# Performance work log

Hardware: AMD Instinct MI355X
Metric: run time of the kernel (lower is better)

## Reference

```python
import jax, jax.numpy as jnp
import numpy as np

B, S, C, V, LAT, NL = 256, 512, 256, 32, 256, 7
DILS = [1, 2, 4, 8, 16, 32, 64]
EPS = 1e-5


def setup_inputs() -> dict:
    key = jax.random.key(0)
    ks = jax.random.split(key, 24)
    s = 0.05
    inp = {
        "x": jax.random.randint(ks[0], (B, S), 0, V, dtype=jnp.int64 if jax.config.read("jax_enable_x64") else jnp.int32),
        "z": jax.random.normal(ks[1], (B, LAT), dtype=jnp.float32),
        "emb": jax.random.normal(ks[2], (V, C), dtype=jnp.float32) * s,
        "latent_W": jax.random.normal(ks[3], (LAT, C), dtype=jnp.float32) * s,
        "latent_b": jnp.zeros((C,), jnp.float32),
        "ln1_g": jnp.ones((NL, C), jnp.float32),
        "ln1_b": jnp.zeros((NL, C), jnp.float32),
        "w1": jax.random.normal(ks[4], (NL, C, C), jnp.float32) * s,
        "b1": jnp.zeros((NL, C), jnp.float32),
        "ln2_g": jnp.ones((NL, C), jnp.float32),
        "ln2_b": jnp.zeros((NL, C), jnp.float32),
        "wd": jax.random.normal(ks[5], (NL, 2, C, C), jnp.float32) * s,  # tap 0 = x[t-d], tap 1 = x[t]
        "bd": jnp.zeros((NL, C), jnp.float32),
        "ln3_g": jnp.ones((NL, C), jnp.float32),
        "ln3_b": jnp.zeros((NL, C), jnp.float32),
        "we": jax.random.normal(ks[6], (NL, C, C), jnp.float32) * s,
        "be": jnp.zeros((NL, C), jnp.float32),
        "wg": jax.random.normal(ks[7], (NL, C, C), jnp.float32) * s,
        "bg": jnp.zeros((NL, C), jnp.float32),
        "out_W": jax.random.normal(ks[8], (C, V), jnp.float32) * s,
        "out_b": jnp.zeros((V,), jnp.float32),
    }
    return inp


def _ln(h, g, b):
    mu = h.mean(-1, keepdims=True)
    var = jnp.mean((h - mu) ** 2, axis=-1, keepdims=True)
    return (h - mu) * jax.lax.rsqrt(var + EPS) * g + b


def _lrelu(h):
    return jnp.where(h >= 0, h, 0.01 * h)


def reference(x, z, emb, latent_W, latent_b, ln1_g, ln1_b, w1, b1,
              ln2_g, ln2_b, wd, bd, ln3_g, ln3_b, we, be, wg, bg,
              out_W, out_b):
    # channel-last layout [B, S, C] throughout (fuses away the torch transposes)
    h = emb[x] + (z @ latent_W + latent_b)[:, None, :]
    for i, d in enumerate(DILS):
        x_inp = h
        t = _lrelu(_ln(x_inp, ln1_g[i], ln1_b[i]))
        t = t @ w1[i] + b1[i]
        t = _lrelu(_ln(t, ln2_g[i], ln2_b[i]))
        # causal dilated conv, kernel=2: out[t] = W0*x[t-d] + W1*x[t]
        t_shift = jnp.pad(t, ((0, 0), (d, 0), (0, 0)))[:, :t.shape[1], :]
        t = t_shift @ wd[i, 0] + t @ wd[i, 1] + bd[i]
        t = _lrelu(_ln(t, ln3_g[i], ln3_b[i]))
        gated = (t @ we[i] + be[i]) * jax.nn.sigmoid(t @ wg[i] + bg[i])
        h = gated + x_inp
    logits = h @ out_W + out_b                      # [B, S, V]
    lp = jax.nn.log_softmax(logits, axis=-1)
    # gather log-prob of next token: lp[:, :-1, :] at x[:, 1:]
    return jnp.take_along_axis(lp[:, :-1, :], x[:, 1:, None], axis=2)[..., 0]
```

## Files before the change

kernel.cpp:

```cpp
#include <hip/hip_runtime.h>

typedef unsigned short u16;
typedef unsigned int   u32;
typedef __attribute__((ext_vector_type(8))) short short8;
typedef __attribute__((ext_vector_type(4))) float f32x4;

struct __align__(8) u16x4 { u16 x, y, z, w; };

#define NL 7
#define M_DIM 131072

#define VMW(N) asm volatile("s_waitcnt vmcnt(" #N ")" ::: "memory")
#define LGW()  asm volatile("s_waitcnt lgkmcnt(0)" ::: "memory")
#define BAR()  __builtin_amdgcn_s_barrier()

__device__ __forceinline__ float b2f(u16 u) {
  union { float f; u32 i; } c; c.i = ((u32)u) << 16; return c.f;
}
__device__ __forceinline__ u16 f2b(float f) {
  union { float f; u32 i; } c; c.f = f;
  u32 r = c.i + 0x7FFFu + ((c.i >> 16) & 1u);
  return (u16)(r >> 16);
}
__device__ __forceinline__ void gload16(const void* g, void* l) {
  __builtin_amdgcn_global_load_lds((const __attribute__((address_space(1))) void*)g,
                                   (__attribute__((address_space(3))) void*)l, 16, 0, 0);
}
__device__ __forceinline__ int xIdx(int row, int chunk) {
  return row * 256 + (((chunk) ^ (row & 7)) << 3);
}


__global__ __launch_bounds__(256) void conv_w1_k(const float* __restrict__ w1, u16* __restrict__ wT) {
  int idx = blockIdx.x * 256 + threadIdx.x;
  int i = idx >> 16, rem = idx & 65535;
  int n = rem >> 8, k = rem & 255;
  wT[idx] = f2b(w1[(i << 16) + (k << 8) + n]);
}

__global__ __launch_bounds__(256) void conv_wd_k(const float* __restrict__ wd, u16* __restrict__ wT) {
  int idx = blockIdx.x * 256 + threadIdx.x;
  int i = idx / 131072, rem = idx & 131071;
  int n = rem >> 9, k2 = rem & 511;
  int tap = k2 >> 8, k = k2 & 255;
  wT[idx] = f2b(wd[(((i * 2 + tap) << 8) + k) * 256 + n]);
}

__global__ __launch_bounds__(256) void conv_weg_k(const float* __restrict__ we, const float* __restrict__ wg,
                                                  u16* __restrict__ wT) {
  int idx = blockIdx.x * 256 + threadIdx.x;
  int i = idx / 131072, rem = idx & 131071;
  int src = rem >> 16, n = (rem >> 8) & 255, k = rem & 255;
  const float* W = src ? wg : we;
  wT[idx] = f2b(W[((i << 8) + k) * 256 + n]);
}

__global__ __launch_bounds__(256) void conv_wo_k(const float* __restrict__ outW, u16* __restrict__ wTo) {
  int idx = blockIdx.x * 256 + threadIdx.x;
  int v = idx >> 8, k = idx & 255;
  wTo[idx] = f2b(outW[k * 32 + v]);
}


__global__ __launch_bounds__(256) void zlat_k(const float* __restrict__ z, const float* __restrict__ W,
                                              const float* __restrict__ bias, float* __restrict__ zlat) {
  int b = blockIdx.x, c = threadIdx.x;
  float acc = bias[c];
  for (int l = 0; l < 256; ++l) acc += z[b * 256 + l] * W[l * 256 + c];
  zlat[b * 256 + c] = acc;
}


__global__ __launch_bounds__(256) void embed_k(const int* __restrict__ x, const float* __restrict__ emb,
                                               const float* __restrict__ zlat, u16* __restrict__ h) {
  int wave = threadIdx.x >> 6, lane = threadIdx.x & 63;
  int r = blockIdx.x * 4 + wave;
  int c = lane * 4;
  int tok = x[r];
  int bi = r >> 9;
  float4 ev = *(const float4*)&emb[tok * 256 + c];
  float4 zv = *(const float4*)&zlat[bi * 256 + c];
  u16x4 hb;
  hb.x = f2b(ev.x + zv.x); hb.y = f2b(ev.y + zv.y);
  hb.z = f2b(ev.z + zv.z); hb.w = f2b(ev.w + zv.w);
  *(u16x4*)&h[(long)r * 256 + c] = hb;
}


__global__ __launch_bounds__(256, 3) void gemm1_k(
    const u16* __restrict__ h, const u16* __restrict__ WT,
    const float* __restrict__ ln1g, const float* __restrict__ ln1b,
    const float* __restrict__ bias,
    const float* __restrict__ ln2g, const float* __restrict__ ln2b,
    u16* __restrict__ V)
{
  __shared__ __align__(16) u16 lA[64 * 256];
  __shared__ __align__(16) u16 lB[256 * 32];
  float* pS  = (float*)lB;
  float* pQ  = (float*)(lB + 512);
  float* muA = (float*)(lB + 1024);
  float* rsA = (float*)(lB + 1152);
  const int tid = threadIdx.x;
  const int lane = tid & 63;
  const int wv = tid >> 6;
  const int wc = wv * 64;
  const int m0 = blockIdx.x * 64;
  const int rA = tid >> 2;
  const int cSw = ((((tid & 3) - ((tid >> 3) & 3)) & 3)) * 8;
  const int lr = lane & 15;
  const int quad = lane >> 4;
  const int sw = ((quad + ((lr >> 1) & 3)) & 3) * 8;

  {
    const int half = lane >> 5, l5 = lane & 31;
    float4 ga = *(const float4*)&ln1g[l5 * 8];
    float4 gb = *(const float4*)&ln1g[l5 * 8 + 4];
    float4 ba = *(const float4*)&ln1b[l5 * 8];
    float4 bb = *(const float4*)&ln1b[l5 * 8 + 4];
    #pragma unroll 4
    for (int it = 0; it < 8; ++it) {
      int row = wv * 16 + it * 2 + half;
      uint4 hv = *(const uint4*)(h + (long)(m0 + row) * 256 + l5 * 8);
      float v0 = b2f((u16)(hv.x & 0xffff)), v1 = b2f((u16)(hv.x >> 16));
      float v2 = b2f((u16)(hv.y & 0xffff)), v3 = b2f((u16)(hv.y >> 16));
      float v4 = b2f((u16)(hv.z & 0xffff)), v5 = b2f((u16)(hv.z >> 16));
      float v6 = b2f((u16)(hv.w & 0xffff)), v7 = b2f((u16)(hv.w >> 16));
      float s = v0 + v1 + v2 + v3 + v4 + v5 + v6 + v7;
      float q = v0*v0 + v1*v1 + v2*v2 + v3*v3 + v4*v4 + v5*v5 + v6*v6 + v7*v7;
      #pragma unroll
      for (int o = 1; o < 32; o <<= 1) { s += __shfl_xor(s, o); q += __shfl_xor(q, o); }
      float mu = s * 0.00390625f;
      float var = q * 0.00390625f - mu * mu;
      float rs = rsqrtf(var + 1e-5f);
      float y0 = (v0 - mu) * rs * ga.x + ba.x; y0 = y0 >= 0.f ? y0 : 0.01f * y0;
      float y1 = (v1 - mu) * rs * ga.y + ba.y; y1 = y1 >= 0.f ? y1 : 0.01f * y1;
      float y2 = (v2 - mu) * rs * ga.z + ba.z; y2 = y2 >= 0.f ? y2 : 0.01f * y2;
      float y3 = (v3 - mu) * rs * ga.w + ba.w; y3 = y3 >= 0.f ? y3 : 0.01f * y3;
      float y4 = (v4 - mu) * rs * gb.x + bb.x; y4 = y4 >= 0.f ? y4 : 0.01f * y4;
      float y5 = (v5 - mu) * rs * gb.y + bb.y; y5 = y5 >= 0.f ? y5 : 0.01f * y5;
      float y6 = (v6 - mu) * rs * gb.z + bb.z; y6 = y6 >= 0.f ? y6 : 0.01f * y6;
      float y7 = (v7 - mu) * rs * gb.w + bb.w; y7 = y7 >= 0.f ? y7 : 0.01f * y7;
      uint4 ov;
      ov.x = (u32)f2b(y0) | ((u32)f2b(y1) << 16);
      ov.y = (u32)f2b(y2) | ((u32)f2b(y3) << 16);
      ov.z = (u32)f2b(y4) | ((u32)f2b(y5) << 16);
      ov.w = (u32)f2b(y6) | ((u32)f2b(y7) << 16);
      *(uint4*)&lA[xIdx(row, l5)] = ov;
    }
  }

  f32x4 acc[4][4];
  #pragma unroll
  for (int i = 0; i < 4; ++i)
    #pragma unroll
    for (int j = 0; j < 4; ++j) {
      acc[i][j][0] = 0.f; acc[i][j][1] = 0.f; acc[i][j][2] = 0.f; acc[i][j][3] = 0.f;
    }

  for (int kt = 0; kt < 8; ++kt) {
    const long bofs = (long)rA * 256 + kt * 32 + cSw;
    #pragma unroll
    for (int j = 0; j < 4; ++j)
      gload16(WT + bofs + (long)(64 * j) * 256, &lB[tid * 8 + j * 2048]);
    __syncthreads();

    short8 af[4], bfr[4];
    #pragma unroll
    for (int mt = 0; mt < 4; ++mt)
      af[mt] = *(const short8*)&lA[xIdx(mt * 16 + lr, 4 * kt + quad)];
    #pragma unroll
    for (int nt = 0; nt < 4; ++nt)
      bfr[nt] = *(const short8*)&lB[(wc + nt * 16 + lr) * 32 + sw];
    #pragma unroll
    for (int mt = 0; mt < 4; ++mt)
      #pragma unroll
      for (int nt = 0; nt < 4; ++nt)
        acc[mt][nt] = __builtin_amdgcn_mfma_f32_16x16x32_bf16(af[mt], bfr[nt], acc[mt][nt], 0, 0, 0);
    __syncthreads();
  }

  float biasv[4], gv[4], bv[4];
  #pragma unroll
  for (int nt = 0; nt < 4; ++nt) {
    int n = wc + nt * 16 + lr;
    biasv[nt] = bias[n]; gv[nt] = ln2g[n]; bv[nt] = ln2b[n];
  }
  #pragma unroll
  for (int mt = 0; mt < 4; ++mt)
    #pragma unroll
    for (int r = 0; r < 4; ++r) {
      float s = 0.f, q = 0.f;
      #pragma unroll
      for (int nt = 0; nt < 4; ++nt) {
        float v = acc[mt][nt][r] + biasv[nt];
        acc[mt][nt][r] = v;
        s += v; q += v * v;
      }
      #pragma unroll
      for (int o = 1; o < 16; o <<= 1) { s += __shfl_xor(s, o); q += __shfl_xor(q, o); }
      if (lr == 0) { pS[(mt * 16 + quad * 4 + r) * 4 + wv] = s; pQ[(mt * 16 + quad * 4 + r) * 4 + wv] = q; }
    }
  __syncthreads();
  if (tid < 64) {
    float S = pS[tid * 4 + 0] + pS[tid * 4 + 1] + pS[tid * 4 + 2] + pS[tid * 4 + 3];
    float Q = pQ[tid * 4 + 0] + pQ[tid * 4 + 1] + pQ[tid * 4 + 2] + pQ[tid * 4 + 3];
    float mu = S * 0.00390625f;
    float var = Q * 0.00390625f - mu * mu;
    muA[tid] = mu; rsA[tid] = rsqrtf(var + 1e-5f);
  }
  __syncthreads();
  #pragma unroll
  for (int mt = 0; mt < 4; ++mt)
    #pragma unroll
    for (int r = 0; r < 4; ++r) {
      int row = mt * 16 + quad * 4 + r;
      float mu = muA[row], rs = rsA[row];
      #pragma unroll
      for (int nt = 0; nt < 4; ++nt) {
        float y = (acc[mt][nt][r] - mu) * rs * gv[nt] + bv[nt];
        y = y >= 0.f ? y : 0.01f * y;
        V[(long)(m0 + row) * 256 + wc + nt * 16 + lr] = f2b(y);
      }
    }
}


__global__ __launch_bounds__(512, 2) void conv_gate_k(
    const u16* __restrict__ A,
    const u16* __restrict__ WTd,
    int dil,
    const float* __restrict__ bd3, const float* __restrict__ g3, const float* __restrict__ bb3,
    const u16* __restrict__ WTe, const u16* __restrict__ WTg,
    const float* __restrict__ bev_, const float* __restrict__ bgv_,
    u16* __restrict__ h)
{
  __shared__ __align__(16) u16 pT[128 * 256];
  __shared__ __align__(16) u16 stg[2][12288];
  float* pS  = (float*)stg[0];
  float* pQ  = (float*)(stg[0] + 1024);
  float* muA = (float*)(stg[0] + 2048);
  float* rsA = (float*)(stg[0] + 2304);

  const int tid = threadIdx.x;
  const int lane = tid & 63;
  const int wv = tid >> 6;
  const int mw = wv >> 2;
  const int nw = wv & 3;
  const int rb = mw * 64;
  const int wc = nw * 64;
  const int m0 = blockIdx.x * 128;
  const int rA = tid >> 2;
  const int cSw = ((((tid & 3) - ((tid >> 3) & 3)) & 3)) * 8;
  const int lr = lane & 15;
  const int quad = lane >> 4;
  const int sw = ((quad + ((lr >> 1) & 3)) & 3) * 8;
  const int mm = m0 + rA;
  const int s1 = mm & 511;
  const short8 zero8 = {0, 0, 0, 0, 0, 0, 0, 0};

  bool zz[4];
  #pragma unroll
  for (int mt = 0; mt < 4; ++mt)
    zz[mt] = ((m0 + rb + mt * 16 + lr) & 511) < dil;

#define STAGE1(KT, BB) do {                                                   \
    const int kt_ = (KT);                                                     \
    const int kk_ = (kt_ & 7) * 32;                                           \
    const int rr_ = (kt_ < 8 && s1 >= dil) ? (mm - dil) : mm;                 \
    gload16(A + (long)rr_ * 256 + kk_ + cSw, &stg[BB][tid * 8]);              \
    const u16* bS_ = WTd + kt_ * 32 + cSw;                                    \
    gload16(bS_ + (long)rA * 512,         &stg[BB][4096 + tid * 8]);          \
    gload16(bS_ + (long)(rA + 128) * 512, &stg[BB][8192 + tid * 8]);          \
  } while (0)
#define STAGEW(WP, KT, BB) do {                                               \
    const long bofs_ = (long)rA * 256 + (KT) * 32 + cSw;                      \
    gload16((WP) + bofs_,              &stg[BB][4096 + tid * 8]);             \
    gload16((WP) + bofs_ + 128L * 256, &stg[BB][8192 + tid * 8]);             \
  } while (0)

  f32x4 acc[4][4];
  #pragma unroll
  for (int i = 0; i < 4; ++i)
    #pragma unroll
    for (int j = 0; j < 4; ++j) {
      acc[i][j][0] = 0.f; acc[i][j][1] = 0.f; acc[i][j][2] = 0.f; acc[i][j][3] = 0.f;
    }

  STAGE1(0, 0);
  STAGE1(1, 1);
  VMW(3);
  BAR();

  #pragma unroll
  for (int r = 0; r < 16; ++r) {
    const int bb = r & 1;
    short8 af[4], bfr[4];
    #pragma unroll
    for (int mt = 0; mt < 4; ++mt) {
      af[mt] = *(const short8*)&stg[bb][(rb + mt * 16 + lr) * 32 + sw];
      if (r < 8 && zz[mt]) af[mt] = zero8;
    }
    #pragma unroll
    for (int nt = 0; nt < 4; ++nt)
      bfr[nt] = *(const short8*)&stg[bb][4096 + (wc + nt * 16 + lr) * 32 + sw];
    LGW();
    BAR();
    if (r <= 13)      STAGE1(r + 2, bb);
    else if (r == 14) STAGEW(WTe, 0, 0);
    else              STAGEW(WTe, 1, 1);
    #pragma unroll
    for (int mt = 0; mt < 4; ++mt)
      #pragma unroll
      for (int nt = 0; nt < 4; ++nt)
        acc[mt][nt] = __builtin_amdgcn_mfma_f32_16x16x32_bf16(af[mt], bfr[nt], acc[mt][nt], 0, 0, 0);
    if (r <= 13)      VMW(3);
    else if (r == 14) VMW(2);
    BAR();
  }

  float b3v[4], g3v[4], o3v[4];
  #pragma unroll
  for (int nt = 0; nt < 4; ++nt) {
    int n = wc + nt * 16 + lr;
    b3v[nt] = bd3[n]; g3v[nt] = g3[n]; o3v[nt] = bb3[n];
  }
  #pragma unroll
  for (int mt = 0; mt < 4; ++mt)
    #pragma unroll
    for (int r = 0; r < 4; ++r) {
      float s = 0.f, q = 0.f;
      #pragma unroll
      for (int nt = 0; nt < 4; ++nt) {
        float v = acc[mt][nt][r] + b3v[nt];
        acc[mt][nt][r] = v;
        s += v; q += v * v;
      }
      #pragma unroll
      for (int o = 1; o < 16; o <<= 1) { s += __shfl_xor(s, o); q += __shfl_xor(q, o); }
      if (lr == 0) {
        int row = rb + mt * 16 + quad * 4 + r;
        pS[row * 4 + nw] = s; pQ[row * 4 + nw] = q;
      }
    }
  LGW(); BAR();
  if (tid < 128) {
    float S = pS[tid * 4 + 0] + pS[tid * 4 + 1] + pS[tid * 4 + 2] + pS[tid * 4 + 3];
    float Q = pQ[tid * 4 + 0] + pQ[tid * 4 + 1] + pQ[tid * 4 + 2] + pQ[tid * 4 + 3];
    float mu = S * 0.00390625f;
    float var = Q * 0.00390625f - mu * mu;
    muA[tid] = mu; rsA[tid] = rsqrtf(var + 1e-5f);
  }
  LGW(); BAR();
  #pragma unroll
  for (int mt = 0; mt < 4; ++mt)
    #pragma unroll
    for (int r = 0; r < 4; ++r) {
      int row = rb + mt * 16 + quad * 4 + r;
      float mu = muA[row], rs = rsA[row];
      #pragma unroll
      for (int nt = 0; nt < 4; ++nt) {
        int col = wc + nt * 16 + lr;
        float y = (acc[mt][nt][r] - mu) * rs * g3v[nt] + o3v[nt];
        y = y >= 0.f ? y : 0.01f * y;
        pT[xIdx(row, col >> 3) + (col & 7)] = f2b(y);
      }
    }
  LGW(); VMW(2); BAR();

  f32x4 accE[4][4], accG[4][4];
  #pragma unroll
  for (int i = 0; i < 4; ++i)
    #pragma unroll
    for (int j = 0; j < 4; ++j) {
      accE[i][j][0] = 0.f; accE[i][j][1] = 0.f; accE[i][j][2] = 0.f; accE[i][j][3] = 0.f;
      accG[i][j][0] = 0.f; accG[i][j][1] = 0.f; accG[i][j][2] = 0.f; accG[i][j][3] = 0.f;
    }

  #pragma unroll
  for (int k = 0; k < 8; ++k) {
    const int bb = k & 1;
    short8 paf[4], bfe[4];
    #pragma unroll
    for (int mt = 0; mt < 4; ++mt)
      paf[mt] = *(const short8*)&pT[xIdx(rb + mt * 16 + lr, 4 * k + quad)];
    #pragma unroll
    for (int nt = 0; nt < 4; ++nt)
      bfe[nt] = *(const short8*)&stg[bb][4096 + (wc + nt * 16 + lr) * 32 + sw];
    LGW(); BAR();
    if (k <= 5)      STAGEW(WTe, k + 2, bb);
    else if (k == 6) STAGEW(WTg, 0, 0);
    else             STAGEW(WTg, 1, 1);
    #pragma unroll
    for (int mt = 0; mt < 4; ++mt)
      #pragma unroll
      for (int nt = 0; nt < 4; ++nt)
        accE[mt][nt] = __builtin_amdgcn_mfma_f32_16x16x32_bf16(paf[mt], bfe[nt], accE[mt][nt], 0, 0, 0);
    VMW(2);
    BAR();
  }

  #pragma unroll
  for (int k = 0; k < 8; ++k) {
    const int bb = k & 1;
    short8 paf[4], bfg[4];
    #pragma unroll
    for (int mt = 0; mt < 4; ++mt)
      paf[mt] = *(const short8*)&pT[xIdx(rb + mt * 16 + lr, 4 * k + quad)];
    #pragma unroll
    for (int nt = 0; nt < 4; ++nt)
      bfg[nt] = *(const short8*)&stg[bb][4096 + (wc + nt * 16 + lr) * 32 + sw];
    LGW(); BAR();
    if (k <= 5) STAGEW(WTg, k + 2, bb);
    #pragma unroll
    for (int mt = 0; mt < 4; ++mt)
      #pragma unroll
      for (int nt = 0; nt < 4; ++nt)
        accG[mt][nt] = __builtin_amdgcn_mfma_f32_16x16x32_bf16(paf[mt], bfg[nt], accG[mt][nt], 0, 0, 0);
    if (k <= 5)      VMW(2);
    else if (k == 6) VMW(0);
    if (k <= 6) BAR();
  }

  float bev[4], bgv[4];
  #pragma unroll
  for (int nt = 0; nt < 4; ++nt) {
    int n = wc + nt * 16 + lr;
    bev[nt] = bev_[n]; bgv[nt] = bgv_[n];
  }
  #pragma unroll
  for (int mt = 0; mt < 4; ++mt)
    #pragma unroll
    for (int r = 0; r < 4; ++r) {
      int row = rb + mt * 16 + quad * 4 + r;
      long off = (long)(m0 + row) * 256;
      #pragma unroll
      for (int nt = 0; nt < 4; ++nt) {
        int n = wc + nt * 16 + lr;
        float e = accE[mt][nt][r] + bev[nt];
        float gg = accG[mt][nt][r] + bgv[nt];
        float hn = e * (1.f / (1.f + expf(-gg))) + b2f(h[off + n]);
        h[off + n] = f2b(hn);
      }
    }
#undef STAGE1
#undef STAGEW
}


__global__ __launch_bounds__(256) void final_k(const u16* __restrict__ h, const u16* __restrict__ WTo,
                                               const float* __restrict__ outb, const int* __restrict__ x,
                                               float* __restrict__ out) {
  __shared__ u16 lW[32 * 264];
  const int tid = threadIdx.x;
  const int lane = tid & 63;
  const int wv = tid >> 6;
  const int mBase = blockIdx.x * 256 + wv * 64;

  #pragma unroll
  for (int j = 0; j < 4; ++j) {
    int chunk = tid + 256 * j;
    int v = chunk >> 5, k8 = chunk & 31;
    uint4 w4 = *(const uint4*)(WTo + v * 256 + k8 * 8);
    *(uint4*)&lW[v * 264 + k8 * 8] = w4;
  }
  __syncthreads();

  const int lq = (lane >> 4) * 8;
  const int lr = lane & 15;
  const int quad = lane >> 4;

  f32x4 acc[4][2];
  #pragma unroll
  for (int mt = 0; mt < 4; ++mt) {
    acc[mt][0][0] = 0.f; acc[mt][0][1] = 0.f; acc[mt][0][2] = 0.f; acc[mt][0][3] = 0.f;
    acc[mt][1][0] = 0.f; acc[mt][1][1] = 0.f; acc[mt][1][2] = 0.f; acc[mt][1][3] = 0.f;
  }

  for (int kt = 0; kt < 8; ++kt) {
    short8 bf0 = *(const short8*)&lW[lr * 264 + kt * 32 + lq];
    short8 bf1 = *(const short8*)&lW[(16 + lr) * 264 + kt * 32 + lq];
    #pragma unroll
    for (int mt = 0; mt < 4; ++mt) {
      short8 af = *(const short8*)(h + (long)(mBase + mt * 16 + lr) * 256 + kt * 32 + lq);
      acc[mt][0] = __builtin_amdgcn_mfma_f32_16x16x32_bf16(af, bf0, acc[mt][0], 0, 0, 0);
      acc[mt][1] = __builtin_amdgcn_mfma_f32_16x16x32_bf16(af, bf1, acc[mt][1], 0, 0, 0);
    }
  }

  float ob0 = outb[lr], ob1 = outb[16 + lr];
  #pragma unroll
  for (int mt = 0; mt < 4; ++mt)
    #pragma unroll
    for (int r = 0; r < 4; ++r) {
      int row = mBase + mt * 16 + quad * 4 + r;
      float lo = acc[mt][0][r] + ob0;
      float hi = acc[mt][1][r] + ob1;
      float mx = fmaxf(lo, hi);
      #pragma unroll
      for (int o = 1; o < 16; o <<= 1) mx = fmaxf(mx, __shfl_xor(mx, o));
      float se = expf(lo - mx) + expf(hi - mx);
      #pragma unroll
      for (int o = 1; o < 16; o <<= 1) se += __shfl_xor(se, o);
      int s = row & 511;
      int xa = (s == 511) ? row : (row + 1);
      int tok = x[xa];
      float lg = (tok < 16) ? lo : hi;
      float lp = lg - mx - logf(se);
      if (s != 511 && lr == (tok & 15))
        out[(row >> 9) * 511 + s] = lp;
    }
}


extern "C" void kernel_launch(void* const* d_in, const int* in_sizes, int n_in,
                              void* d_out, int out_size, void* d_ws, size_t ws_size,
                              hipStream_t stream) {
  const int*   x    = (const int*)d_in[0];
  const float* z    = (const float*)d_in[1];
  const float* emb  = (const float*)d_in[2];
  const float* latW = (const float*)d_in[3];
  const float* latb = (const float*)d_in[4];
  const float* ln1g = (const float*)d_in[5];
  const float* ln1b = (const float*)d_in[6];
  const float* w1   = (const float*)d_in[7];
  const float* b1   = (const float*)d_in[8];
  const float* ln2g = (const float*)d_in[9];
  const float* ln2b = (const float*)d_in[10];
  const float* wd   = (const float*)d_in[11];
  const float* bd   = (const float*)d_in[12];
  const float* ln3g = (const float*)d_in[13];
  const float* ln3b = (const float*)d_in[14];
  const float* we   = (const float*)d_in[15];
  const float* be   = (const float*)d_in[16];
  const float* wg   = (const float*)d_in[17];
  const float* bg   = (const float*)d_in[18];
  const float* outW = (const float*)d_in[19];
  const float* outb = (const float*)d_in[20];

  char* ws = (char*)d_ws;
  u16*   h    = (u16*)(ws + 0);
  u16*   bufA = (u16*)(ws + 67108864);
  float* zlat = (float*)(ws + 201326592);
  u16*   wT1  = (u16*)(ws + 201588736);
  u16*   wTd  = (u16*)(ws + 202506240);
  u16*   wTeg = (u16*)(ws + 204341248);
  u16*   wTo  = (u16*)(ws + 206176256);

  conv_w1_k <<<1792, 256, 0, stream>>>(w1, wT1);
  conv_wd_k <<<3584, 256, 0, stream>>>(wd, wTd);
  conv_weg_k<<<3584, 256, 0, stream>>>(we, wg, wTeg);
  conv_wo_k <<<32, 256, 0, stream>>>(outW, wTo);
  zlat_k    <<<256, 256, 0, stream>>>(z, latW, latb, zlat);
  embed_k   <<<M_DIM / 4, 256, 0, stream>>>(x, emb, zlat, h);

  for (int i = 0; i < NL; ++i) {
    int d = 1 << i;
    gemm1_k<<<M_DIM / 64, 256, 0, stream>>>(
        h, wT1 + i * 65536, ln1g + i * 256, ln1b + i * 256, b1 + i * 256,
        ln2g + i * 256, ln2b + i * 256, bufA);
    conv_gate_k<<<M_DIM / 128, 512, 0, stream>>>(
        bufA, wTd + i * 131072, d,
        bd + i * 256, ln3g + i * 256, ln3b + i * 256,
        wTeg + i * 131072, wTeg + i * 131072 + 65536,
        be + i * 256, bg + i * 256, h);
  }

  final_k<<<M_DIM / 256, 256, 0, stream>>>(h, wTo, outb, x, (float*)d_out);
}
```

Baseline: 1.411 ms.

## Triple-buffer conv_gate staging with split-phase loads and MFMA priority

Rewrites the conv_gate_k main loops to use three LDS staging buffers instead of two, prefetching two tiles ahead. Each tile is split into two halves, with global-to-LDS loads interleaved between them, sched_barrier fences and s_setprio raised around the MFMA clusters. The LayerNorm scratch arrays get their own LDS instead of aliasing the staging buffer. The aim is to overlap memory traffic with matrix math and keep waves from stalling on each other, at the cost of more LDS per block, which may cut occupancy, and more barriers per tile.

```diff
diff --git a/kernel.cpp b/kernel.cpp
--- a/kernel.cpp
+++ b/kernel.cpp
@@ -13,6 +13,10 @@
 #define VMW(N) asm volatile("s_waitcnt vmcnt(" #N ")" ::: "memory")
 #define LGW()  asm volatile("s_waitcnt lgkmcnt(0)" ::: "memory")
 #define BAR()  __builtin_amdgcn_s_barrier()
+#define SB0()  __builtin_amdgcn_sched_barrier(0)
+#define PRIO1  __builtin_amdgcn_s_setprio(1)
+#define PRIO0  __builtin_amdgcn_s_setprio(0)
+#define MFMA   __builtin_amdgcn_mfma_f32_16x16x32_bf16
 
 __device__ __forceinline__ float b2f(u16 u) {
   union { float f; u32 i; } c; c.i = ((u32)u) << 16; return c.f;
@@ -175,7 +179,7 @@
     for (int mt = 0; mt < 4; ++mt)
       #pragma unroll
       for (int nt = 0; nt < 4; ++nt)
-        acc[mt][nt] = __builtin_amdgcn_mfma_f32_16x16x32_bf16(af[mt], bfr[nt], acc[mt][nt], 0, 0, 0);
+        acc[mt][nt] = MFMA(af[mt], bfr[nt], acc[mt][nt], 0, 0, 0);
     __syncthreads();
   }
 
@@ -235,11 +239,9 @@
     u16* __restrict__ h)
 {
   __shared__ __align__(16) u16 pT[128 * 256];
-  __shared__ __align__(16) u16 stg[2][12288];
-  float* pS  = (float*)stg[0];
-  float* pQ  = (float*)(stg[0] + 1024);
-  float* muA = (float*)(stg[0] + 2048);
-  float* rsA = (float*)(stg[0] + 2304);
+  __shared__ __align__(16) u16 stg[3][12288];
+  __shared__ float pS[128][4], pQ[128][4];
+  __shared__ float muA[128], rsA[128];
 
   const int tid = threadIdx.x;
   const int lane = tid & 63;
@@ -263,20 +265,24 @@
   for (int mt = 0; mt < 4; ++mt)
     zz[mt] = ((m0 + rb + mt * 16 + lr) & 511) < dil;
 
-#define STAGE1(KT, BB) do {                                                   \
-    const int kt_ = (KT);                                                     \
-    const int kk_ = (kt_ & 7) * 32;                                           \
-    const int rr_ = (kt_ < 8 && s1 >= dil) ? (mm - dil) : mm;                 \
-    gload16(A + (long)rr_ * 256 + kk_ + cSw, &stg[BB][tid * 8]);              \
-    const u16* bS_ = WTd + kt_ * 32 + cSw;                                    \
-    gload16(bS_ + (long)rA * 512,         &stg[BB][4096 + tid * 8]);          \
-    gload16(bS_ + (long)(rA + 128) * 512, &stg[BB][8192 + tid * 8]);          \
-  } while (0)
-#define STAGEW(WP, KT, BB) do {                                               \
-    const long bofs_ = (long)rA * 256 + (KT) * 32 + cSw;                      \
-    gload16((WP) + bofs_,              &stg[BB][4096 + tid * 8]);             \
-    gload16((WP) + bofs_ + 128L * 256, &stg[BB][8192 + tid * 8]);             \
-  } while (0)
+  const int rowA0 = (s1 >= dil) ? (mm - dil) : mm;
+  const u16* pA0 = A + (long)rowA0 * 256 + cSw;
+  const u16* pA1 = A + (long)mm * 256 + cSw;
+  const u16* pWd = WTd + (long)rA * 512 + cSw;
+  const u16* pWe = WTe + (long)rA * 256 + cSw;
+  const u16* pWg = WTg + (long)rA * 256 + cSw;
+
+  auto stA   = [&](int kt, int nb) {
+    const u16* pa = (kt < 8 ? pA0 : pA1) + (kt & 7) * 32;
+    gload16(pa, &stg[nb][tid * 8]);
+  };
+  auto stW1a = [&](int kt, int nb) { gload16(pWd + kt * 32,             &stg[nb][4096 + tid * 8]); };
+  auto stW1b = [&](int kt, int nb) { gload16(pWd + 128 * 512 + kt * 32, &stg[nb][8192 + tid * 8]); };
+  auto stW2a = [&](const u16* pw, int j, int nb) { gload16(pw + j * 32,             &stg[nb][4096 + tid * 8]); };
+  auto stW2b = [&](const u16* pw, int j, int nb) { gload16(pw + 128 * 256 + j * 32, &stg[nb][8192 + tid * 8]); };
+  auto rdA = [&](int bb, int mt) -> short8 { return *(const short8*)&stg[bb][(rb + mt * 16 + lr) * 32 + sw]; };
+  auto rdB = [&](int bb, int nt) -> short8 { return *(const short8*)&stg[bb][4096 + (wc + nt * 16 + lr) * 32 + sw]; };
+  auto rdP = [&](int j, int mt) -> short8 { return *(const short8*)&pT[xIdx(rb + mt * 16 + lr, 4 * j + quad)]; };
 
   f32x4 acc[4][4];
   #pragma unroll
@@ -286,86 +292,105 @@
       acc[i][j][0] = 0.f; acc[i][j][1] = 0.f; acc[i][j][2] = 0.f; acc[i][j][3] = 0.f;
     }
 
-  STAGE1(0, 0);
-  STAGE1(1, 1);
+  auto p1_tile = [&](int t) {
+    const int bb = t % 3, nb = (t + 2) % 3;
+    const bool tap0 = t < 8;
+    short8 af0 = rdA(bb, 0), af1 = rdA(bb, 1);
+    short8 b0 = rdB(bb, 0), b1 = rdB(bb, 1), b2 = rdB(bb, 2), b3 = rdB(bb, 3);
+    if (tap0) { if (zz[0]) af0 = zero8; if (zz[1]) af1 = zero8; }
+    BAR();
+    if (t <= 13) { stA(t + 2, nb); stW1a(t + 2, nb); }
+    else         { stW2a(pWe, t - 14, nb); }
+    LGW(); SB0();
+    PRIO1;
+    acc[0][0] = MFMA(af0, b0, acc[0][0], 0, 0, 0);
+    acc[0][1] = MFMA(af0, b1, acc[0][1], 0, 0, 0);
+    acc[0][2] = MFMA(af0, b2, acc[0][2], 0, 0, 0);
+    acc[0][3] = MFMA(af0, b3, acc[0][3], 0, 0, 0);
+    acc[1][0] = MFMA(af1, b0, acc[1][0], 0, 0, 0);
+    acc[1][1] = MFMA(af1, b1, acc[1][1], 0, 0, 0);
+    acc[1][2] = MFMA(af1, b2, acc[1][2], 0, 0, 0);
+    acc[1][3] = MFMA(af1, b3, acc[1][3], 0, 0, 0);
+    PRIO0;
+    BAR();
+    short8 af2 = rdA(bb, 2), af3 = rdA(bb, 3);
+    if (tap0) { if (zz[2]) af2 = zero8; if (zz[3]) af3 = zero8; }
+    BAR();
+    if (t <= 13) { stW1b(t + 2, nb); }
+    else         { stW2b(pWe, t - 14, nb); }
+    LGW(); SB0();
+    PRIO1;
+    acc[2][0] = MFMA(af2, b0, acc[2][0], 0, 0, 0);
+    acc[2][1] = MFMA(af2, b1, acc[2][1], 0, 0, 0);
+    acc[2][2] = MFMA(af2, b2, acc[2][2], 0, 0, 0);
+    acc[2][3] = MFMA(af2, b3, acc[2][3], 0, 0, 0);
+    acc[3][0] = MFMA(af3, b0, acc[3][0], 0, 0, 0);
+    acc[3][1] = MFMA(af3, b1, acc[3][1], 0, 0, 0);
+    acc[3][2] = MFMA(af3, b2, acc[3][2], 0, 0, 0);
+    acc[3][3] = MFMA(af3, b3, acc[3][3], 0, 0, 0);
+    PRIO0;
+  };
+
+  stA(0, 0); stW1a(0, 0); stW1b(0, 0);
+  stA(1, 1); stW1a(1, 1); stW1b(1, 1);
   VMW(3);
   BAR();
 
   #pragma unroll
-  for (int r = 0; r < 16; ++r) {
-    const int bb = r & 1;
-    short8 af[4], bfr[4];
-    #pragma unroll
-    for (int mt = 0; mt < 4; ++mt) {
-      af[mt] = *(const short8*)&stg[bb][(rb + mt * 16 + lr) * 32 + sw];
-      if (r < 8 && zz[mt]) af[mt] = zero8;
-    }
-    #pragma unroll
-    for (int nt = 0; nt < 4; ++nt)
-      bfr[nt] = *(const short8*)&stg[bb][4096 + (wc + nt * 16 + lr) * 32 + sw];
-    LGW();
-    BAR();
-    if (r <= 13)      STAGE1(r + 2, bb);
-    else if (r == 14) STAGEW(WTe, 0, 0);
-    else              STAGEW(WTe, 1, 1);
+  for (int t = 0; t <= 13; ++t) { p1_tile(t); VMW(3); BAR(); }
+  p1_tile(14); VMW(2); BAR();
+  p1_tile(15); VMW(2); BAR();
+
+  {
+    float b3v[4], g3v[4], o3v[4];
+    #pragma unroll
+    for (int nt = 0; nt < 4; ++nt) {
+      int n = wc + nt * 16 + lr;
+      b3v[nt] = bd3[n]; g3v[nt] = g3[n]; o3v[nt] = bb3[n];
+    }
     #pragma unroll
     for (int mt = 0; mt < 4; ++mt)
       #pragma unroll
-      for (int nt = 0; nt < 4; ++nt)
-        acc[mt][nt] = __builtin_amdgcn_mfma_f32_16x16x32_bf16(af[mt], bfr[nt], acc[mt][nt], 0, 0, 0);
-    if (r <= 13)      VMW(3);
-    else if (r == 14) VMW(2);
-    BAR();
-  }
-
-  float b3v[4], g3v[4], o3v[4];
-  #pragma unroll
-  for (int nt = 0; nt < 4; ++nt) {
-    int n = wc + nt * 16 + lr;
-    b3v[nt] = bd3[n]; g3v[nt] = g3[n]; o3v[nt] = bb3[n];
-  }
-  #pragma unroll
-  for (int mt = 0; mt < 4; ++mt)
-    #pragma unroll
-    for (int r = 0; r < 4; ++r) {
-      float s = 0.f, q = 0.f;
-      #pragma unroll
-      for (int nt = 0; nt < 4; ++nt) {
-        float v = acc[mt][nt][r] + b3v[nt];
-        acc[mt][nt][r] = v;
-        s += v; q += v * v;
+      for (int r = 0; r < 4; ++r) {
+        float s = 0.f, q = 0.f;
+        #pragma unroll
+        for (int nt = 0; nt < 4; ++nt) {
+          float v = acc[mt][nt][r] + b3v[nt];
+          acc[mt][nt][r] = v;
+          s += v; q += v * v;
+        }
+        #pragma unroll
+        for (int o = 1; o < 16; o <<= 1) { s += __shfl_xor(s, o); q += __shfl_xor(q, o); }
+        if (lr == 0) {
+          int row = rb + mt * 16 + quad * 4 + r;
+          pS[row][nw] = s; pQ[row][nw] = q;
+        }
       }
-      #pragma unroll
-      for (int o = 1; o < 16; o <<= 1) { s += __shfl_xor(s, o); q += __shfl_xor(q, o); }
-      if (lr == 0) {
+    LGW(); BAR();
+    if (tid < 128) {
+      float S = pS[tid][0] + pS[tid][1] + pS[tid][2] + pS[tid][3];
+      float Q = pQ[tid][0] + pQ[tid][1] + pQ[tid][2] + pQ[tid][3];
+      float mu = S * 0.00390625f;
+      float var = Q * 0.00390625f - mu * mu;
+      muA[tid] = mu; rsA[tid] = rsqrtf(var + 1e-5f);
+    }
+    LGW(); BAR();
+    #pragma unroll
+    for (int mt = 0; mt < 4; ++mt)
+      #pragma unroll
+      for (int r = 0; r < 4; ++r) {
         int row = rb + mt * 16 + quad * 4 + r;
-        pS[row * 4 + nw] = s; pQ[row * 4 + nw] = q;
+        float mu = muA[row], rs = rsA[row];
+        #pragma unroll
+        for (int nt = 0; nt < 4; ++nt) {
+          int col = wc + nt * 16 + lr;
+          float y = (acc[mt][nt][r] - mu) * rs * g3v[nt] + o3v[nt];
+          y = y >= 0.f ? y : 0.01f * y;
+          pT[xIdx(row, col >> 3) + (col & 7)] = f2b(y);
+        }
       }
-    }
-  LGW(); BAR();
-  if (tid < 128) {
-    float S = pS[tid * 4 + 0] + pS[tid * 4 + 1] + pS[tid * 4 + 2] + pS[tid * 4 + 3];
-    float Q = pQ[tid * 4 + 0] + pQ[tid * 4 + 1] + pQ[tid * 4 + 2] + pQ[tid * 4 + 3];
-    float mu = S * 0.00390625f;
-    float var = Q * 0.00390625f - mu * mu;
-    muA[tid] = mu; rsA[tid] = rsqrtf(var + 1e-5f);
-  }
-  LGW(); BAR();
-  #pragma unroll
-  for (int mt = 0; mt < 4; ++mt)
-    #pragma unroll
-    for (int r = 0; r < 4; ++r) {
-      int row = rb + mt * 16 + quad * 4 + r;
-      float mu = muA[row], rs = rsA[row];
-      #pragma unroll
-      for (int nt = 0; nt < 4; ++nt) {
-        int col = wc + nt * 16 + lr;
-        float y = (acc[mt][nt][r] - mu) * rs * g3v[nt] + o3v[nt];
-        y = y >= 0.f ? y : 0.01f * y;
-        pT[xIdx(row, col >> 3) + (col & 7)] = f2b(y);
-      }
-    }
-  LGW(); VMW(2); BAR();
+    LGW(); BAR();
+  }
 
   f32x4 accE[4][4], accG[4][4];
   #pragma unroll
@@ -376,50 +401,48 @@
       accG[i][j][0] = 0.f; accG[i][j][1] = 0.f; accG[i][j][2] = 0.f; accG[i][j][3] = 0.f;
     }
 
-  #pragma unroll
-  for (int k = 0; k < 8; ++k) {
-    const int bb = k & 1;
-    short8 paf[4], bfe[4];
-    #pragma unroll
-    for (int mt = 0; mt < 4; ++mt)
-      paf[mt] = *(const short8*)&pT[xIdx(rb + mt * 16 + lr, 4 * k + quad)];
-    #pragma unroll
-    for (int nt = 0; nt < 4; ++nt)
-      bfe[nt] = *(const short8*)&stg[bb][4096 + (wc + nt * 16 + lr) * 32 + sw];
-    LGW(); BAR();
-    if (k <= 5)      STAGEW(WTe, k + 2, bb);
-    else if (k == 6) STAGEW(WTg, 0, 0);
-    else             STAGEW(WTg, 1, 1);
-    #pragma unroll
-    for (int mt = 0; mt < 4; ++mt)
-      #pragma unroll
-      for (int nt = 0; nt < 4; ++nt)
-        accE[mt][nt] = __builtin_amdgcn_mfma_f32_16x16x32_bf16(paf[mt], bfe[nt], accE[mt][nt], 0, 0, 0);
-    VMW(2);
+  auto p2_tile = [&](int t, int j, f32x4 (&ac)[4][4], const u16* stSrc, int stJ, int nloads) {
+    const int bb = t % 3, nb = (t + 2) % 3;
+    short8 p0 = rdP(j, 0), p1 = rdP(j, 1);
+    short8 w0 = rdB(bb, 0), w1 = rdB(bb, 1), w2 = rdB(bb, 2), w3 = rdB(bb, 3);
     BAR();
-  }
-
-  #pragma unroll
-  for (int k = 0; k < 8; ++k) {
-    const int bb = k & 1;
-    short8 paf[4], bfg[4];
-    #pragma unroll
-    for (int mt = 0; mt < 4; ++mt)
-      paf[mt] = *(const short8*)&pT[xIdx(rb + mt * 16 + lr, 4 * k + quad)];
-    #pragma unroll
-    for (int nt = 0; nt < 4; ++nt)
-      bfg[nt] = *(const short8*)&stg[bb][4096 + (wc + nt * 16 + lr) * 32 + sw];
-    LGW(); BAR();
-    if (k <= 5) STAGEW(WTg, k + 2, bb);
-    #pragma unroll
-    for (int mt = 0; mt < 4; ++mt)
-      #pragma unroll
-      for (int nt = 0; nt < 4; ++nt)
-        accG[mt][nt] = __builtin_amdgcn_mfma_f32_16x16x32_bf16(paf[mt], bfg[nt], accG[mt][nt], 0, 0, 0);
-    if (k <= 5)      VMW(2);
-    else if (k == 6) VMW(0);
-    if (k <= 6) BAR();
-  }
+    if (nloads) stW2a(stSrc, stJ, nb);
+    LGW(); SB0();
+    PRIO1;
+    ac[0][0] = MFMA(p0, w0, ac[0][0], 0, 0, 0);
+    ac[0][1] = MFMA(p0, w1, ac[0][1], 0, 0, 0);
+    ac[0][2] = MFMA(p0, w2, ac[0][2], 0, 0, 0);
+    ac[0][3] = MFMA(p0, w3, ac[0][3], 0, 0, 0);
+    ac[1][0] = MFMA(p1, w0, ac[1][0], 0, 0, 0);
+    ac[1][1] = MFMA(p1, w1, ac[1][1], 0, 0, 0);
+    ac[1][2] = MFMA(p1, w2, ac[1][2], 0, 0, 0);
+    ac[1][3] = MFMA(p1, w3, ac[1][3], 0, 0, 0);
+    PRIO0;
+    BAR();
+    short8 p2 = rdP(j, 2), p3 = rdP(j, 3);
+    BAR();
+    if (nloads) stW2b(stSrc, stJ, nb);
+    LGW(); SB0();
+    PRIO1;
+    ac[2][0] = MFMA(p2, w0, ac[2][0], 0, 0, 0);
+    ac[2][1] = MFMA(p2, w1, ac[2][1], 0, 0, 0);
+    ac[2][2] = MFMA(p2, w2, ac[2][2], 0, 0, 0);
+    ac[2][3] = MFMA(p2, w3, ac[2][3], 0, 0, 0);
+    ac[3][0] = MFMA(p3, w0, ac[3][0], 0, 0, 0);
+    ac[3][1] = MFMA(p3, w1, ac[3][1], 0, 0, 0);
+    ac[3][2] = MFMA(p3, w2, ac[3][2], 0, 0, 0);
+    ac[3][3] = MFMA(p3, w3, ac[3][3], 0, 0, 0);
+    PRIO0;
+  };
+
+  #pragma unroll
+  for (int t = 16; t <= 21; ++t) { p2_tile(t, t - 16, accE, pWe, t - 14, 1); VMW(2); BAR(); }
+  p2_tile(22, 6, accE, pWg, 0, 1); VMW(2); BAR();
+  p2_tile(23, 7, accE, pWg, 1, 1); VMW(2); BAR();
+  #pragma unroll
+  for (int t = 24; t <= 29; ++t) { p2_tile(t, t - 24, accG, pWg, t - 22, 1); VMW(2); BAR(); }
+  p2_tile(30, 6, accG, pWg, 0, 0); VMW(0); BAR();
+  p2_tile(31, 7, accG, pWg, 0, 0);
 
   float bev[4], bgv[4];
   #pragma unroll
@@ -442,8 +465,6 @@
         h[off + n] = f2b(hn);
       }
     }
-#undef STAGE1
-#undef STAGEW
 }
 
 
@@ -482,8 +503,8 @@
     #pragma unroll
     for (int mt = 0; mt < 4; ++mt) {
       short8 af = *(const short8*)(h + (long)(mBase + mt * 16 + lr) * 256 + kt * 32 + lq);
-      acc[mt][0] = __builtin_amdgcn_mfma_f32_16x16x32_bf16(af, bf0, acc[mt][0], 0, 0, 0);
-      acc[mt][1] = __builtin_amdgcn_mfma_f32_16x16x32_bf16(af, bf1, acc[mt][1], 0, 0, 0);
+      acc[mt][0] = MFMA(af, bf0, acc[mt][0], 0, 0, 0);
+      acc[mt][1] = MFMA(af, bf1, acc[mt][1], 0, 0, 0);
     }
   }
 
```

Result: no change. 1.434 ms (+1.6%).
